# Kernel optimization log

Hardware: AMD Instinct MI355X
Metric: run time of the kernel (lower is better)

## Reference

```python
import jax, jax.numpy as jnp
import numpy as np

N_NODES = 50000
N_EDGES = 800000
IN_C, HID_C, OUT_C = 512, 256, 128


def setup_inputs() -> dict:
    key = jax.random.key(0)
    k1, k2, k3, k4, k5, k6 = jax.random.split(key, 6)
    x = jax.random.normal(k1, (N_NODES, IN_C), dtype=jnp.float32)
    edge_index = jax.random.randint(k2, (2, N_EDGES), 0, N_NODES, dtype=jnp.int64)
    # Glorot-ish init for linear weights, zero bias (PyG GCNConv default)
    W1 = jax.random.normal(k3, (IN_C, HID_C), dtype=jnp.float32) / np.sqrt(IN_C)
    b1 = jnp.zeros((HID_C,), dtype=jnp.float32)
    W2 = jax.random.normal(k4, (HID_C, OUT_C), dtype=jnp.float32) / np.sqrt(HID_C)
    b2 = jnp.zeros((OUT_C,), dtype=jnp.float32)
    return {"x": x, "edge_index": edge_index, "W1": W1, "b1": b1, "W2": W2, "b2": b2}


def _gcn_layer(h, src, dst, norm, W, b, n_nodes):
    # h: [N, Fin] -> [N, Fout];  out_i = sum_{j->i} norm_e * (h W)_j + b
    h = h @ W
    msg = h[src] * norm[:, None]            # [E+N, Fout]
    out = jax.ops.segment_sum(msg, dst, num_segments=n_nodes)
    return out + b


def reference(x, edge_index, W1, b1, W2, b2):
    n = x.shape[0]
    loops = jnp.arange(n, dtype=edge_index.dtype)
    src = jnp.concatenate([edge_index[0], loops])  # add self-loops
    dst = jnp.concatenate([edge_index[1], loops])
    # symmetric normalization D^{-1/2} (A+I) D^{-1/2}
    deg = jax.ops.segment_sum(jnp.ones_like(src, dtype=x.dtype), dst, num_segments=n)
    dinv = jax.lax.rsqrt(jnp.maximum(deg, 1.0))
    norm = dinv[src] * dinv[dst]

    h = _gcn_layer(x, src, dst, norm, W1, b1, n)
    h = jax.nn.relu(h)
    # dropout: identity in eval mode (training=False)
    out = _gcn_layer(h, src, dst, norm, W2, b2, n)
    return out
```

## Files before the change

kernel.cpp:

```cpp
#include <hip/hip_runtime.h>
#include <hip/hip_bf16.h>

#define N_NODES 50000
#define N_EDGES 800000
#define IN_C 512
#define HID_C 256
#define OUT_C 128
#define SCAN_BLOCKS 49

typedef short bf16x8 __attribute__((ext_vector_type(8)));
typedef float f32x4 __attribute__((ext_vector_type(4)));
typedef float f32x2 __attribute__((ext_vector_type(2)));

__device__ __forceinline__ float bf2f(unsigned short u) {
    return __uint_as_float(((unsigned)u) << 16);
}
__device__ __forceinline__ unsigned short f2bf(float f) {
    __hip_bfloat16 h = __float2bfloat16(f);
    return *(unsigned short*)&h;
}
__device__ __forceinline__ void acc_fp8x4(int dw, float* a) {
    f32x2 lo = __builtin_amdgcn_cvt_pk_f32_fp8(dw, false);
    f32x2 hi = __builtin_amdgcn_cvt_pk_f32_fp8(dw, true);
    a[0] += lo[0]; a[1] += lo[1]; a[2] += hi[0]; a[3] += hi[1];
}
__device__ __forceinline__ unsigned char f2fp8(float f) {
    return (unsigned char)(__builtin_amdgcn_cvt_pk_fp8_f32(f, 0.0f, 0, false) & 0xff);
}

__global__ void zero_counts_kernel(int* __restrict__ counts) {
    int i = blockIdx.x * blockDim.x + threadIdx.x;
    if (i < N_NODES) counts[i] = 0;
}

__global__ void count_kernel(const int* __restrict__ ei, int* __restrict__ counts) {
    int e = blockIdx.x * blockDim.x + threadIdx.x;
    if (e < N_EDGES) atomicAdd(&counts[ei[N_EDGES + e]], 1);
}

__global__ __launch_bounds__(256) void scan_part_kernel(const int* __restrict__ counts,
                                                        int* __restrict__ excl,
                                                        int* __restrict__ bsums) {
    __shared__ int tsum[256];
    const int t = threadIdx.x;
    const int base = blockIdx.x * 1024 + t * 4;
    int v[4];
    int s = 0;
#pragma unroll
    for (int j = 0; j < 4; j++) {
        int idx = base + j;
        v[j] = (idx < N_NODES) ? counts[idx] : 0;
        s += v[j];
    }
    tsum[t] = s;
    __syncthreads();
    for (int off = 1; off < 256; off <<= 1) {
        int add = (t >= off) ? tsum[t - off] : 0;
        __syncthreads();
        tsum[t] += add;
        __syncthreads();
    }
    int run = tsum[t] - s;
#pragma unroll
    for (int j = 0; j < 4; j++) {
        int idx = base + j;
        if (idx < N_NODES) excl[idx] = run;
        run += v[j];
    }
    if (t == 255) bsums[blockIdx.x] = tsum[255];
}

__global__ void scan_sums_kernel(int* __restrict__ bsums) {
    int ln = threadIdx.x;
    int v = (ln < SCAN_BLOCKS) ? bsums[ln] : 0;
    for (int off = 1; off < 64; off <<= 1) {
        int u = __shfl_up(v, off, 64);
        if (ln >= off) v += u;
    }
    int excl = __shfl_up(v, 1, 64);
    if (ln == 0) excl = 0;
    if (ln < SCAN_BLOCKS) bsums[ln] = excl;
}

__global__ void add_dinv_kernel(int* __restrict__ offsets, const int* __restrict__ bsums,
                                int* __restrict__ woff, const int* __restrict__ counts,
                                float* __restrict__ dinv) {
    int i = blockIdx.x * blockDim.x + threadIdx.x;
    if (i < N_NODES) {
        int o = offsets[i] + bsums[i >> 10];
        offsets[i] = o;
        woff[i] = o;
        dinv[i] = rsqrtf(1.0f + (float)counts[i]);
    }
    if (i == 0) offsets[N_NODES] = N_EDGES;
}

__global__ void fill_kernel(const int* __restrict__ ei, int* __restrict__ woff,
                            int* __restrict__ sedge) {
    int e = blockIdx.x * blockDim.x + threadIdx.x;
    if (e < N_EDGES) {
        int s = ei[e];
        int d = ei[N_EDGES + e];
        int pos = atomicAdd(&woff[d], 1);
        sedge[pos] = s;
    }
}

__global__ __launch_bounds__(256) void cast_x_kernel(const float* __restrict__ x,
                                                     unsigned short* __restrict__ xb) {
    size_t i = ((size_t)blockIdx.x * 256 + threadIdx.x) * 4;
    float4 v = *(const float4*)&x[i];
    ushort4 o;
    o.x = f2bf(v.x); o.y = f2bf(v.y); o.z = f2bf(v.z); o.w = f2bf(v.w);
    *(ushort4*)&xb[i] = o;
}

__global__ __launch_bounds__(256) void tcast_kernel(const float* __restrict__ W,
                                                    unsigned short* __restrict__ WT,
                                                    int K, int N) {
    int idx = blockIdx.x * 256 + threadIdx.x;
    int n = idx / K, k = idx - n * K;
    WT[idx] = f2bf(W[(size_t)k * N + n]);
}

template <bool FP8_OUT>
__global__ __launch_bounds__(256) void mfma_gemm_bt(const unsigned short* __restrict__ A,
                                                    const unsigned short* __restrict__ BT,
                                                    void* __restrict__ Cv,
                                                    const float* __restrict__ dinv,
                                                    int M, int N, int K) {
    __shared__ unsigned short As[128 * 32];
    __shared__ unsigned short Bs[128 * 32];

    const int tid = threadIdx.x;
    const int w = tid >> 6;
    const int ln = tid & 63;
    const int br = blockIdx.y * 128;
    const int bc = blockIdx.x * 128;

    const int quad = ln >> 4;
    const int l16 = ln & 15;
    const int wr = (w >> 1) * 64;
    const int wc = (w & 1) * 64;

    const int crow = ln >> 2;
    const int koff = (ln & 3) * 8;

    f32x4 acc[4][4];
#pragma unroll
    for (int mt = 0; mt < 4; mt++)
#pragma unroll
        for (int nt = 0; nt < 4; nt++) acc[mt][nt] = (f32x4){0.f, 0.f, 0.f, 0.f};

    for (int kk = 0; kk < K; kk += 32) {
#pragma unroll
        for (int t = 0; t < 2; t++) {
            int c = w + t * 4;
            int row = br + c * 16 + crow;
            row = row < M ? row : M - 1;
            const unsigned short* gp = A + (size_t)row * K + kk + koff;
            unsigned short* lp = As + c * 512 + ln * 8;
            __builtin_amdgcn_global_load_lds((const __attribute__((address_space(1))) void*)gp,
                                             (__attribute__((address_space(3))) void*)lp,
                                             16, 0, 0);
        }
#pragma unroll
        for (int t = 0; t < 2; t++) {
            int c = w + t * 4;
            int row = bc + c * 16 + crow;
            const unsigned short* gp = BT + (size_t)row * K + kk + koff;
            unsigned short* lp = Bs + c * 512 + ln * 8;
            __builtin_amdgcn_global_load_lds((const __attribute__((address_space(1))) void*)gp,
                                             (__attribute__((address_space(3))) void*)lp,
                                             16, 0, 0);
        }
        __syncthreads();

        bf16x8 af[4], bfr[4];
#pragma unroll
        for (int mt = 0; mt < 4; mt++)
            af[mt] = *(const bf16x8*)&As[(wr + mt * 16 + l16) * 32 + quad * 8];
#pragma unroll
        for (int nt = 0; nt < 4; nt++)
            bfr[nt] = *(const bf16x8*)&Bs[(wc + nt * 16 + l16) * 32 + quad * 8];
#pragma unroll
        for (int mt = 0; mt < 4; mt++)
#pragma unroll
            for (int nt = 0; nt < 4; nt++)
                acc[mt][nt] = __builtin_amdgcn_mfma_f32_16x16x32_bf16(af[mt], bfr[nt],
                                                                      acc[mt][nt], 0, 0, 0);
        __syncthreads();
    }

#pragma unroll
    for (int mt = 0; mt < 4; mt++) {
#pragma unroll
        for (int r = 0; r < 4; r++) {
            int gr = br + wr + mt * 16 + quad * 4 + r;
            if (gr < M) {
                float ds = dinv[gr];
#pragma unroll
                for (int nt = 0; nt < 4; nt++) {
                    int gc = bc + wc + nt * 16 + l16;
                    float v = ds * acc[mt][nt][r];
                    if (FP8_OUT)
                        ((unsigned char*)Cv)[(size_t)gr * N + gc] = f2fp8(v);
                    else
                        ((unsigned short*)Cv)[(size_t)gr * N + gc] = f2bf(v);
                }
            }
        }
    }
}

__global__ __launch_bounds__(256) void gather1_fp8(const int* __restrict__ offsets,
                                                   const int* __restrict__ sedge,
                                                   const unsigned char* __restrict__ H,
                                                   const float* __restrict__ dinv,
                                                   const float* __restrict__ bias,
                                                   unsigned short* __restrict__ out) {
    const int node = blockIdx.x * 4 + (threadIdx.x >> 6);
    if (node >= N_NODES) return;
    const int ln = threadIdx.x & 63;
    const int g = ln >> 5;
    const int l = ln & 31;
    const int c0 = l * 8;

    float acc[8] = {};
    if (g == 0) {
        uint2 d = *(const uint2*)&H[(size_t)node * HID_C + c0];
        acc_fp8x4((int)d.x, acc);
        acc_fp8x4((int)d.y, acc + 4);
    }

    int k = offsets[node] + g;
    const int k1 = offsets[node + 1];
    for (; k + 6 < k1; k += 8) {
        int s0 = sedge[k], s1 = sedge[k + 2], s2 = sedge[k + 4], s3 = sedge[k + 6];
        uint2 d0 = *(const uint2*)&H[(size_t)s0 * HID_C + c0];
        uint2 d1 = *(const uint2*)&H[(size_t)s1 * HID_C + c0];
        uint2 d2 = *(const uint2*)&H[(size_t)s2 * HID_C + c0];
        uint2 d3 = *(const uint2*)&H[(size_t)s3 * HID_C + c0];
        acc_fp8x4((int)d0.x, acc); acc_fp8x4((int)d0.y, acc + 4);
        acc_fp8x4((int)d1.x, acc); acc_fp8x4((int)d1.y, acc + 4);
        acc_fp8x4((int)d2.x, acc); acc_fp8x4((int)d2.y, acc + 4);
        acc_fp8x4((int)d3.x, acc); acc_fp8x4((int)d3.y, acc + 4);
    }
    for (; k < k1; k += 2) {
        int s0 = sedge[k];
        uint2 d0 = *(const uint2*)&H[(size_t)s0 * HID_C + c0];
        acc_fp8x4((int)d0.x, acc);
        acc_fp8x4((int)d0.y, acc + 4);
    }

#pragma unroll
    for (int j = 0; j < 8; j++) acc[j] += __shfl_xor(acc[j], 32, 64);

    if (g == 0) {
        const float di = dinv[node];
        bf16x8 o;
#pragma unroll
        for (int j = 0; j < 8; j++)
            o[j] = (short)f2bf(fmaxf(di * acc[j] + bias[c0 + j], 0.0f));
        *(bf16x8*)&out[(size_t)node * HID_C + c0] = o;
    }
}

__global__ __launch_bounds__(256) void gather2_bf16(const int* __restrict__ offsets,
                                                    const int* __restrict__ sedge,
                                                    const unsigned short* __restrict__ H,
                                                    const float* __restrict__ dinv,
                                                    const float* __restrict__ bias,
                                                    float* __restrict__ out) {
    const int node = blockIdx.x * 4 + (threadIdx.x >> 6);
    if (node >= N_NODES) return;
    const int ln = threadIdx.x & 63;
    const int g = ln >> 4;
    const int l = ln & 15;
    const int c0 = l * 8;

    float acc[8] = {};
    if (g == 0) {
        bf16x8 h = *(const bf16x8*)&H[(size_t)node * OUT_C + c0];
#pragma unroll
        for (int j = 0; j < 8; j++) acc[j] = bf2f((unsigned short)h[j]);
    }

    int k = offsets[node] + g;
    const int k1 = offsets[node + 1];
    for (; k + 12 < k1; k += 16) {
        int s0 = sedge[k], s1 = sedge[k + 4], s2 = sedge[k + 8], s3 = sedge[k + 12];
        bf16x8 h0 = *(const bf16x8*)&H[(size_t)s0 * OUT_C + c0];
        bf16x8 h1 = *(const bf16x8*)&H[(size_t)s1 * OUT_C + c0];
        bf16x8 h2 = *(const bf16x8*)&H[(size_t)s2 * OUT_C + c0];
        bf16x8 h3 = *(const bf16x8*)&H[(size_t)s3 * OUT_C + c0];
#pragma unroll
        for (int j = 0; j < 8; j++) {
            acc[j] += bf2f((unsigned short)h0[j]);
            acc[j] += bf2f((unsigned short)h1[j]);
            acc[j] += bf2f((unsigned short)h2[j]);
            acc[j] += bf2f((unsigned short)h3[j]);
        }
    }
    for (; k < k1; k += 4) {
        int s0 = sedge[k];
        bf16x8 h0 = *(const bf16x8*)&H[(size_t)s0 * OUT_C + c0];
#pragma unroll
        for (int j = 0; j < 8; j++) acc[j] += bf2f((unsigned short)h0[j]);
    }

#pragma unroll
    for (int m = 16; m < 64; m <<= 1) {
#pragma unroll
        for (int j = 0; j < 8; j++) acc[j] += __shfl_xor(acc[j], m, 64);
    }

    if (g == 0) {
        const float di = dinv[node];
        float o[8];
#pragma unroll
        for (int j = 0; j < 8; j++) o[j] = di * acc[j] + bias[c0 + j];
        *(float4*)&out[(size_t)node * OUT_C + c0] = make_float4(o[0], o[1], o[2], o[3]);
        *(float4*)&out[(size_t)node * OUT_C + c0 + 4] = make_float4(o[4], o[5], o[6], o[7]);
    }
}

extern "C" void kernel_launch(void* const* d_in, const int* in_sizes, int n_in,
                              void* d_out, int out_size, void* d_ws, size_t ws_size,
                              hipStream_t stream) {
    const float* x  = (const float*)d_in[0];
    const int*   ei = (const int*)d_in[1];
    const float* W1 = (const float*)d_in[2];
    const float* b1 = (const float*)d_in[3];
    const float* W2 = (const float*)d_in[4];
    const float* b2 = (const float*)d_in[5];
    float* out = (float*)d_out;

    int*   counts     = (int*)d_ws;
    int*   offsets    = counts + 50048;
    int*   woff       = offsets + 50052;
    int*   bsums      = woff + 50048;
    float* dinv       = (float*)(bsums + 64);
    int*   sedge      = (int*)(dinv + 50048);
    unsigned short* W1T = (unsigned short*)(sedge + 800000);
    unsigned short* W2T = W1T + 131072;
    unsigned short* xb  = W2T + 32768;
    unsigned char*  H1  = (unsigned char*)(xb + (size_t)N_NODES * IN_C);
    unsigned short* A1b = xb;
    unsigned short* H2  = xb + (size_t)N_NODES * HID_C;

    zero_counts_kernel<<<(N_NODES + 255) / 256, 256, 0, stream>>>(counts);
    count_kernel<<<(N_EDGES + 255) / 256, 256, 0, stream>>>(ei, counts);
    scan_part_kernel<<<SCAN_BLOCKS, 256, 0, stream>>>(counts, offsets, bsums);
    scan_sums_kernel<<<1, 64, 0, stream>>>(bsums);
    add_dinv_kernel<<<(N_NODES + 255) / 256, 256, 0, stream>>>(offsets, bsums, woff, counts, dinv);
    fill_kernel<<<(N_EDGES + 255) / 256, 256, 0, stream>>>(ei, woff, sedge);

    cast_x_kernel<<<(N_NODES * IN_C) / 1024, 256, 0, stream>>>(x, xb);
    tcast_kernel<<<(IN_C * HID_C) / 256, 256, 0, stream>>>(W1, W1T, IN_C, HID_C);
    tcast_kernel<<<(HID_C * OUT_C) / 256, 256, 0, stream>>>(W2, W2T, HID_C, OUT_C);

    {
        dim3 grid(HID_C / 128, (N_NODES + 127) / 128);
        mfma_gemm_bt<true><<<grid, 256, 0, stream>>>(xb, W1T, (void*)H1, dinv,
                                                     N_NODES, HID_C, IN_C);
    }
    gather1_fp8<<<(N_NODES + 3) / 4, 256, 0, stream>>>(offsets, sedge, H1, dinv, b1, A1b);

    {
        dim3 grid(OUT_C / 128, (N_NODES + 127) / 128);
        mfma_gemm_bt<false><<<grid, 256, 0, stream>>>(A1b, W2T, (void*)H2, dinv,
                                                      N_NODES, OUT_C, HID_C);
    }
    gather2_bf16<<<(N_NODES + 3) / 4, 256, 0, stream>>>(offsets, sedge, H2, dinv, b2, out);
}
```

Measured before the change: 403.3 us.

## Fuse fp32-to-bf16 cast of x into first GEMM with full-width N tile

Removes the separate cast_x kernel and has the first GEMM read fp32 x directly, converting to bf16 while staging the A tile into shared memory. The new kernel uses 64-row blocks that span all 256 output columns, so each x row is read once and W1 is staged through direct global-to-LDS loads. This avoids writing and re-reading a 50 MB bf16 copy of x, at the cost of less latency hiding in the A-tile loads and smaller M tiles.

```diff
diff --git a/kernel.cpp b/kernel.cpp
--- a/kernel.cpp
+++ b/kernel.cpp
@@ -106,15 +106,6 @@
     }
 }
 
-__global__ __launch_bounds__(256) void cast_x_kernel(const float* __restrict__ x,
-                                                     unsigned short* __restrict__ xb) {
-    size_t i = ((size_t)blockIdx.x * 256 + threadIdx.x) * 4;
-    float4 v = *(const float4*)&x[i];
-    ushort4 o;
-    o.x = f2bf(v.x); o.y = f2bf(v.y); o.z = f2bf(v.z); o.w = f2bf(v.w);
-    *(ushort4*)&xb[i] = o;
-}
-
 __global__ __launch_bounds__(256) void tcast_kernel(const float* __restrict__ W,
                                                     unsigned short* __restrict__ WT,
                                                     int K, int N) {
@@ -123,10 +114,91 @@
     WT[idx] = f2bf(W[(size_t)k * N + n]);
 }
 
-template <bool FP8_OUT>
+__global__ __launch_bounds__(256) void gemm1_fused(const float* __restrict__ x,
+                                                   const unsigned short* __restrict__ BT,
+                                                   unsigned char* __restrict__ C,
+                                                   const float* __restrict__ dinv) {
+    __shared__ unsigned short As[64 * 32];
+    __shared__ unsigned short Bs[256 * 32];
+
+    const int tid = threadIdx.x;
+    const int w = tid >> 6;
+    const int ln = tid & 63;
+    const int br = blockIdx.x * 64;
+
+    const int quad = ln >> 4;
+    const int l16 = ln & 15;
+    const int wc = w * 64;
+
+    const int ar = tid >> 2;
+    const int ak = (tid & 3) * 8;
+
+    int arow = br + ar;
+    arow = arow < N_NODES ? arow : N_NODES - 1;
+    const float* xrow = x + (size_t)arow * IN_C + ak;
+
+    f32x4 acc[4][4];
+#pragma unroll
+    for (int mt = 0; mt < 4; mt++)
+#pragma unroll
+        for (int nt = 0; nt < 4; nt++) acc[mt][nt] = (f32x4){0.f, 0.f, 0.f, 0.f};
+
+    for (int kk = 0; kk < IN_C; kk += 32) {
+        float4 v0 = *(const float4*)(xrow + kk);
+        float4 v1 = *(const float4*)(xrow + kk + 4);
+        bf16x8 a8;
+        a8[0] = (short)f2bf(v0.x); a8[1] = (short)f2bf(v0.y);
+        a8[2] = (short)f2bf(v0.z); a8[3] = (short)f2bf(v0.w);
+        a8[4] = (short)f2bf(v1.x); a8[5] = (short)f2bf(v1.y);
+        a8[6] = (short)f2bf(v1.z); a8[7] = (short)f2bf(v1.w);
+        *(bf16x8*)&As[ar * 32 + ak] = a8;
+#pragma unroll
+        for (int t = 0; t < 4; t++) {
+            int n = (tid >> 2) + 64 * t;
+            const unsigned short* gp = BT + (size_t)n * IN_C + kk + ak;
+            unsigned short* lp = Bs + t * 2048 + tid * 8;
+            __builtin_amdgcn_global_load_lds((const __attribute__((address_space(1))) void*)gp,
+                                             (__attribute__((address_space(3))) void*)lp,
+                                             16, 0, 0);
+        }
+        __syncthreads();
+
+        bf16x8 af[4], bfr[4];
+#pragma unroll
+        for (int mt = 0; mt < 4; mt++)
+            af[mt] = *(const bf16x8*)&As[(mt * 16 + l16) * 32 + quad * 8];
+#pragma unroll
+        for (int nt = 0; nt < 4; nt++)
+            bfr[nt] = *(const bf16x8*)&Bs[(wc + nt * 16 + l16) * 32 + quad * 8];
+#pragma unroll
+        for (int mt = 0; mt < 4; mt++)
+#pragma unroll
+            for (int nt = 0; nt < 4; nt++)
+                acc[mt][nt] = __builtin_amdgcn_mfma_f32_16x16x32_bf16(af[mt], bfr[nt],
+                                                                      acc[mt][nt], 0, 0, 0);
+        __syncthreads();
+    }
+
+#pragma unroll
+    for (int mt = 0; mt < 4; mt++) {
+#pragma unroll
+        for (int r = 0; r < 4; r++) {
+            int gr = br + mt * 16 + quad * 4 + r;
+            if (gr < N_NODES) {
+                float ds = dinv[gr];
+#pragma unroll
+                for (int nt = 0; nt < 4; nt++) {
+                    int gc = wc + nt * 16 + l16;
+                    C[(size_t)gr * HID_C + gc] = f2fp8(ds * acc[mt][nt][r]);
+                }
+            }
+        }
+    }
+}
+
 __global__ __launch_bounds__(256) void mfma_gemm_bt(const unsigned short* __restrict__ A,
                                                     const unsigned short* __restrict__ BT,
-                                                    void* __restrict__ Cv,
+                                                    unsigned short* __restrict__ C,
                                                     const float* __restrict__ dinv,
                                                     int M, int N, int K) {
     __shared__ unsigned short As[128 * 32];
@@ -202,11 +274,7 @@
 #pragma unroll
                 for (int nt = 0; nt < 4; nt++) {
                     int gc = bc + wc + nt * 16 + l16;
-                    float v = ds * acc[mt][nt][r];
-                    if (FP8_OUT)
-                        ((unsigned char*)Cv)[(size_t)gr * N + gc] = f2fp8(v);
-                    else
-                        ((unsigned short*)Cv)[(size_t)gr * N + gc] = f2bf(v);
+                    C[(size_t)gr * N + gc] = f2bf(ds * acc[mt][nt][r]);
                 }
             }
         }
@@ -356,21 +424,15 @@
     add_dinv_kernel<<<(N_NODES + 255) / 256, 256, 0, stream>>>(offsets, bsums, woff, counts, dinv);
     fill_kernel<<<(N_EDGES + 255) / 256, 256, 0, stream>>>(ei, woff, sedge);
 
-    cast_x_kernel<<<(N_NODES * IN_C) / 1024, 256, 0, stream>>>(x, xb);
     tcast_kernel<<<(IN_C * HID_C) / 256, 256, 0, stream>>>(W1, W1T, IN_C, HID_C);
     tcast_kernel<<<(HID_C * OUT_C) / 256, 256, 0, stream>>>(W2, W2T, HID_C, OUT_C);
 
-    {
-        dim3 grid(HID_C / 128, (N_NODES + 127) / 128);
-        mfma_gemm_bt<true><<<grid, 256, 0, stream>>>(xb, W1T, (void*)H1, dinv,
-                                                     N_NODES, HID_C, IN_C);
-    }
+    gemm1_fused<<<(N_NODES + 63) / 64, 256, 0, stream>>>(x, W1T, H1, dinv);
     gather1_fp8<<<(N_NODES + 3) / 4, 256, 0, stream>>>(offsets, sedge, H1, dinv, b1, A1b);
 
     {
         dim3 grid(OUT_C / 128, (N_NODES + 127) / 128);
-        mfma_gemm_bt<false><<<grid, 256, 0, stream>>>(A1b, W2T, (void*)H2, dinv,
-                                                      N_NODES, OUT_C, HID_C);
+        mfma_gemm_bt<<<grid, 256, 0, stream>>>(A1b, W2T, H2, dinv, N_NODES, OUT_C, HID_C);
     }
     gather2_bf16<<<(N_NODES + 3) / 4, 256, 0, stream>>>(offsets, sedge, H2, dinv, b2, out);
 }
```

Result: faster. 386.2 us (-4.3%).

## Fuse x bf16 cast into GEMM1 and use register-fed MFMA with pre-packed weights

Applied to the files above, without the earlier changes.

Removes the separate x-to-bf16 cast kernel by having GEMM1 read fp32 rows of x directly and convert them in registers. Weights are pre-packed into the MFMA B-fragment layout so each lane loads its fragment straight from global memory. Both GEMMs drop the LDS tiling and barriers, and each wave computes a 16-row by full-width output strip. This saves a full write and read of the 50000x512 bf16 copy of x, but B fragments are now re-read from global/L2 by every wave with no LDS reuse, and the larger accumulator arrays raise register pressure.

```diff
diff --git a/kernel.cpp b/kernel.cpp
--- a/kernel.cpp
+++ b/kernel.cpp
@@ -106,109 +106,129 @@
     }
 }
 
-__global__ __launch_bounds__(256) void cast_x_kernel(const float* __restrict__ x,
-                                                     unsigned short* __restrict__ xb) {
-    size_t i = ((size_t)blockIdx.x * 256 + threadIdx.x) * 4;
-    float4 v = *(const float4*)&x[i];
-    ushort4 o;
-    o.x = f2bf(v.x); o.y = f2bf(v.y); o.z = f2bf(v.z); o.w = f2bf(v.w);
-    *(ushort4*)&xb[i] = o;
-}
-
-__global__ __launch_bounds__(256) void tcast_kernel(const float* __restrict__ W,
-                                                    unsigned short* __restrict__ WT,
-                                                    int K, int N) {
+__global__ __launch_bounds__(256) void pack_w_kernel(const float* __restrict__ W,
+                                                     unsigned short* __restrict__ Bp,
+                                                     int N) {
     int idx = blockIdx.x * 256 + threadIdx.x;
-    int n = idx / K, k = idx - n * K;
-    WT[idx] = f2bf(W[(size_t)k * N + n]);
-}
-
-template <bool FP8_OUT>
-__global__ __launch_bounds__(256) void mfma_gemm_bt(const unsigned short* __restrict__ A,
-                                                    const unsigned short* __restrict__ BT,
-                                                    void* __restrict__ Cv,
-                                                    const float* __restrict__ dinv,
-                                                    int M, int N, int K) {
-    __shared__ unsigned short As[128 * 32];
-    __shared__ unsigned short Bs[128 * 32];
-
-    const int tid = threadIdx.x;
-    const int w = tid >> 6;
-    const int ln = tid & 63;
-    const int br = blockIdx.y * 128;
-    const int bc = blockIdx.x * 128;
-
+    int j = idx & 7;
+    int ln = (idx >> 3) & 63;
+    int rest = idx >> 9;
+    int NT = N >> 4;
+    int nt = rest % NT, t = rest / NT;
+    int k = t * 32 + (ln >> 4) * 8 + j;
+    int n = nt * 16 + (ln & 15);
+    Bp[idx] = f2bf(W[(size_t)k * N + n]);
+}
+
+__global__ __launch_bounds__(256) void gemm1_rf(const float* __restrict__ x,
+                                                const unsigned short* __restrict__ Bp,
+                                                unsigned char* __restrict__ C,
+                                                const float* __restrict__ dinv) {
+    const int w = threadIdx.x >> 6;
+    const int ln = threadIdx.x & 63;
     const int quad = ln >> 4;
     const int l16 = ln & 15;
-    const int wr = (w >> 1) * 64;
-    const int wc = (w & 1) * 64;
-
-    const int crow = ln >> 2;
-    const int koff = (ln & 3) * 8;
-
-    f32x4 acc[4][4];
-#pragma unroll
-    for (int mt = 0; mt < 4; mt++)
-#pragma unroll
-        for (int nt = 0; nt < 4; nt++) acc[mt][nt] = (f32x4){0.f, 0.f, 0.f, 0.f};
-
-    for (int kk = 0; kk < K; kk += 32) {
-#pragma unroll
-        for (int t = 0; t < 2; t++) {
-            int c = w + t * 4;
-            int row = br + c * 16 + crow;
-            row = row < M ? row : M - 1;
-            const unsigned short* gp = A + (size_t)row * K + kk + koff;
-            unsigned short* lp = As + c * 512 + ln * 8;
-            __builtin_amdgcn_global_load_lds((const __attribute__((address_space(1))) void*)gp,
-                                             (__attribute__((address_space(3))) void*)lp,
-                                             16, 0, 0);
+    const int rbase = blockIdx.x * 64 + w * 16;
+
+    int arow = rbase + l16;
+    arow = arow < N_NODES ? arow : N_NODES - 1;
+    const float* xr = x + (size_t)arow * IN_C + quad * 8;
+    const unsigned short* bl = Bp + ln * 8;
+
+    f32x4 acc[16];
+#pragma unroll
+    for (int nt = 0; nt < 16; nt++) acc[nt] = (f32x4){0.f, 0.f, 0.f, 0.f};
+
+    for (int t = 0; t < 16; t++) {
+        float4 v0 = *(const float4*)(xr + t * 32);
+        float4 v1 = *(const float4*)(xr + t * 32 + 4);
+        bf16x8 a8;
+        a8[0] = (short)f2bf(v0.x); a8[1] = (short)f2bf(v0.y);
+        a8[2] = (short)f2bf(v0.z); a8[3] = (short)f2bf(v0.w);
+        a8[4] = (short)f2bf(v1.x); a8[5] = (short)f2bf(v1.y);
+        a8[6] = (short)f2bf(v1.z); a8[7] = (short)f2bf(v1.w);
+        const unsigned short* bs = bl + t * 16 * 512;
+#pragma unroll
+        for (int h = 0; h < 2; h++) {
+            bf16x8 b0 = *(const bf16x8*)(bs + (h * 8 + 0) * 512);
+            bf16x8 b1 = *(const bf16x8*)(bs + (h * 8 + 1) * 512);
+            bf16x8 b2 = *(const bf16x8*)(bs + (h * 8 + 2) * 512);
+            bf16x8 b3 = *(const bf16x8*)(bs + (h * 8 + 3) * 512);
+            bf16x8 b4 = *(const bf16x8*)(bs + (h * 8 + 4) * 512);
+            bf16x8 b5 = *(const bf16x8*)(bs + (h * 8 + 5) * 512);
+            bf16x8 b6 = *(const bf16x8*)(bs + (h * 8 + 6) * 512);
+            bf16x8 b7 = *(const bf16x8*)(bs + (h * 8 + 7) * 512);
+            acc[h * 8 + 0] = __builtin_amdgcn_mfma_f32_16x16x32_bf16(a8, b0, acc[h * 8 + 0], 0, 0, 0);
+            acc[h * 8 + 1] = __builtin_amdgcn_mfma_f32_16x16x32_bf16(a8, b1, acc[h * 8 + 1], 0, 0, 0);
+            acc[h * 8 + 2] = __builtin_amdgcn_mfma_f32_16x16x32_bf16(a8, b2, acc[h * 8 + 2], 0, 0, 0);
+            acc[h * 8 + 3] = __builtin_amdgcn_mfma_f32_16x16x32_bf16(a8, b3, acc[h * 8 + 3], 0, 0, 0);
+            acc[h * 8 + 4] = __builtin_amdgcn_mfma_f32_16x16x32_bf16(a8, b4, acc[h * 8 + 4], 0, 0, 0);
+            acc[h * 8 + 5] = __builtin_amdgcn_mfma_f32_16x16x32_bf16(a8, b5, acc[h * 8 + 5], 0, 0, 0);
+            acc[h * 8 + 6] = __builtin_amdgcn_mfma_f32_16x16x32_bf16(a8, b6, acc[h * 8 + 6], 0, 0, 0);
+            acc[h * 8 + 7] = __builtin_amdgcn_mfma_f32_16x16x32_bf16(a8, b7, acc[h * 8 + 7], 0, 0, 0);
         }
-#pragma unroll
-        for (int t = 0; t < 2; t++) {
-            int c = w + t * 4;
-            int row = bc + c * 16 + crow;
-            const unsigned short* gp = BT + (size_t)row * K + kk + koff;
-            unsigned short* lp = Bs + c * 512 + ln * 8;
-            __builtin_amdgcn_global_load_lds((const __attribute__((address_space(1))) void*)gp,
-                                             (__attribute__((address_space(3))) void*)lp,
-                                             16, 0, 0);
+    }
+
+#pragma unroll
+    for (int r = 0; r < 4; r++) {
+        int gr = rbase + quad * 4 + r;
+        if (gr < N_NODES) {
+            float ds = dinv[gr];
+#pragma unroll
+            for (int nt = 0; nt < 16; nt++)
+                C[(size_t)gr * HID_C + nt * 16 + l16] = f2fp8(ds * acc[nt][r]);
         }
-        __syncthreads();
-
-        bf16x8 af[4], bfr[4];
-#pragma unroll
-        for (int mt = 0; mt < 4; mt++)
-            af[mt] = *(const bf16x8*)&As[(wr + mt * 16 + l16) * 32 + quad * 8];
-#pragma unroll
-        for (int nt = 0; nt < 4; nt++)
-            bfr[nt] = *(const bf16x8*)&Bs[(wc + nt * 16 + l16) * 32 + quad * 8];
-#pragma unroll
-        for (int mt = 0; mt < 4; mt++)
-#pragma unroll
-            for (int nt = 0; nt < 4; nt++)
-                acc[mt][nt] = __builtin_amdgcn_mfma_f32_16x16x32_bf16(af[mt], bfr[nt],
-                                                                      acc[mt][nt], 0, 0, 0);
-        __syncthreads();
-    }
-
-#pragma unroll
-    for (int mt = 0; mt < 4; mt++) {
-#pragma unroll
-        for (int r = 0; r < 4; r++) {
-            int gr = br + wr + mt * 16 + quad * 4 + r;
-            if (gr < M) {
-                float ds = dinv[gr];
-#pragma unroll
-                for (int nt = 0; nt < 4; nt++) {
-                    int gc = bc + wc + nt * 16 + l16;
-                    float v = ds * acc[mt][nt][r];
-                    if (FP8_OUT)
-                        ((unsigned char*)Cv)[(size_t)gr * N + gc] = f2fp8(v);
-                    else
-                        ((unsigned short*)Cv)[(size_t)gr * N + gc] = f2bf(v);
-                }
-            }
+    }
+}
+
+__global__ __launch_bounds__(256) void gemm2_rf(const unsigned short* __restrict__ A,
+                                                const unsigned short* __restrict__ Bp,
+                                                unsigned short* __restrict__ C,
+                                                const float* __restrict__ dinv) {
+    const int w = threadIdx.x >> 6;
+    const int ln = threadIdx.x & 63;
+    const int quad = ln >> 4;
+    const int l16 = ln & 15;
+    const int rbase = blockIdx.x * 64 + w * 16;
+
+    int arow = rbase + l16;
+    arow = arow < N_NODES ? arow : N_NODES - 1;
+    const unsigned short* ar = A + (size_t)arow * HID_C + quad * 8;
+    const unsigned short* bl = Bp + ln * 8;
+
+    f32x4 acc[8];
+#pragma unroll
+    for (int nt = 0; nt < 8; nt++) acc[nt] = (f32x4){0.f, 0.f, 0.f, 0.f};
+
+    for (int t = 0; t < 8; t++) {
+        bf16x8 a8 = *(const bf16x8*)(ar + t * 32);
+        const unsigned short* bs = bl + t * 8 * 512;
+        bf16x8 b0 = *(const bf16x8*)(bs + 0 * 512);
+        bf16x8 b1 = *(const bf16x8*)(bs + 1 * 512);
+        bf16x8 b2 = *(const bf16x8*)(bs + 2 * 512);
+        bf16x8 b3 = *(const bf16x8*)(bs + 3 * 512);
+        bf16x8 b4 = *(const bf16x8*)(bs + 4 * 512);
+        bf16x8 b5 = *(const bf16x8*)(bs + 5 * 512);
+        bf16x8 b6 = *(const bf16x8*)(bs + 6 * 512);
+        bf16x8 b7 = *(const bf16x8*)(bs + 7 * 512);
+        acc[0] = __builtin_amdgcn_mfma_f32_16x16x32_bf16(a8, b0, acc[0], 0, 0, 0);
+        acc[1] = __builtin_amdgcn_mfma_f32_16x16x32_bf16(a8, b1, acc[1], 0, 0, 0);
+        acc[2] = __builtin_amdgcn_mfma_f32_16x16x32_bf16(a8, b2, acc[2], 0, 0, 0);
+        acc[3] = __builtin_amdgcn_mfma_f32_16x16x32_bf16(a8, b3, acc[3], 0, 0, 0);
+        acc[4] = __builtin_amdgcn_mfma_f32_16x16x32_bf16(a8, b4, acc[4], 0, 0, 0);
+        acc[5] = __builtin_amdgcn_mfma_f32_16x16x32_bf16(a8, b5, acc[5], 0, 0, 0);
+        acc[6] = __builtin_amdgcn_mfma_f32_16x16x32_bf16(a8, b6, acc[6], 0, 0, 0);
+        acc[7] = __builtin_amdgcn_mfma_f32_16x16x32_bf16(a8, b7, acc[7], 0, 0, 0);
+    }
+
+#pragma unroll
+    for (int r = 0; r < 4; r++) {
+        int gr = rbase + quad * 4 + r;
+        if (gr < N_NODES) {
+            float ds = dinv[gr];
+#pragma unroll
+            for (int nt = 0; nt < 8; nt++)
+                C[(size_t)gr * OUT_C + nt * 16 + l16] = f2bf(ds * acc[nt][r]);
         }
     }
 }
@@ -342,9 +362,9 @@
     int*   bsums      = woff + 50048;
     float* dinv       = (float*)(bsums + 64);
     int*   sedge      = (int*)(dinv + 50048);
-    unsigned short* W1T = (unsigned short*)(sedge + 800000);
-    unsigned short* W2T = W1T + 131072;
-    unsigned short* xb  = W2T + 32768;
+    unsigned short* Bp1 = (unsigned short*)(sedge + 800000);
+    unsigned short* Bp2 = Bp1 + 131072;
+    unsigned short* xb  = Bp2 + 32768;
     unsigned char*  H1  = (unsigned char*)(xb + (size_t)N_NODES * IN_C);
     unsigned short* A1b = xb;
     unsigned short* H2  = xb + (size_t)N_NODES * HID_C;
@@ -356,21 +376,12 @@
     add_dinv_kernel<<<(N_NODES + 255) / 256, 256, 0, stream>>>(offsets, bsums, woff, counts, dinv);
     fill_kernel<<<(N_EDGES + 255) / 256, 256, 0, stream>>>(ei, woff, sedge);
 
-    cast_x_kernel<<<(N_NODES * IN_C) / 1024, 256, 0, stream>>>(x, xb);
-    tcast_kernel<<<(IN_C * HID_C) / 256, 256, 0, stream>>>(W1, W1T, IN_C, HID_C);
-    tcast_kernel<<<(HID_C * OUT_C) / 256, 256, 0, stream>>>(W2, W2T, HID_C, OUT_C);
-
-    {
-        dim3 grid(HID_C / 128, (N_NODES + 127) / 128);
-        mfma_gemm_bt<true><<<grid, 256, 0, stream>>>(xb, W1T, (void*)H1, dinv,
-                                                     N_NODES, HID_C, IN_C);
-    }
+    pack_w_kernel<<<(IN_C * HID_C) / 256, 256, 0, stream>>>(W1, Bp1, HID_C);
+    pack_w_kernel<<<(HID_C * OUT_C) / 256, 256, 0, stream>>>(W2, Bp2, OUT_C);
+
+    gemm1_rf<<<(N_NODES + 63) / 64, 256, 0, stream>>>(x, Bp1, H1, dinv);
     gather1_fp8<<<(N_NODES + 3) / 4, 256, 0, stream>>>(offsets, sedge, H1, dinv, b1, A1b);
 
-    {
-        dim3 grid(OUT_C / 128, (N_NODES + 127) / 128);
-        mfma_gemm_bt<false><<<grid, 256, 0, stream>>>(A1b, W2T, (void*)H2, dinv,
-                                                      N_NODES, OUT_C, HID_C);
-    }
+    gemm2_rf<<<(N_NODES + 63) / 64, 256, 0, stream>>>(A1b, Bp2, H2, dinv);
     gather2_bf16<<<(N_NODES + 3) / 4, 256, 0, stream>>>(offsets, sedge, H2, dinv, b2, out);
 }
```

Result: no change. 399.0 us (-1.1%).
